# Performance work log

Hardware: AMD Instinct MI355X
Metric: run time of the kernel (lower is better)

Reference implementation:

```python
import jax, jax.numpy as jnp
import numpy as np

B, S, H = 8, 1024, 1024
NH, HD = 16, 64
EPS = 1e-12


def _p(w, g):
    # make_p_layer: w + gamma * clamp(w, min=0)
    return w + g * jnp.clip(w, 0.0, None)


def _pproc(x, W, b, g):
    # z = layer(x); zp = player(x); return zp * (z/zp).detach()  (value == z)
    z = x @ W.T + b
    zp = x @ _p(W, g).T + _p(b, g)
    return zp * jax.lax.stop_gradient(z / zp)


def _ln_nowb_detach(x):
    # 'nowb' LayerNorm (no weight/bias), mean and std detached (LNargsDetach)
    m = jax.lax.stop_gradient(jnp.mean(x, axis=-1, keepdims=True))
    v = jax.lax.stop_gradient(jnp.var(x, axis=-1, keepdims=True))
    return (x - m) / jnp.sqrt(v + EPS)


def setup_inputs() -> dict:
    key = jax.random.key(0)
    ks = jax.random.split(key, 10)
    lin = lambda k: (jax.random.normal(k, (H, H), jnp.float32) * 0.02)
    vec = lambda k: (jax.random.normal(k, (H,), jnp.float32) * 0.02)
    return {
        "hidden_states": jax.random.normal(ks[0], (B, S, H), jnp.float32),
        "Wq": lin(ks[1]), "bq": vec(ks[2]),
        "Wk": lin(ks[3]), "bk": vec(ks[4]),
        "Wv": lin(ks[5]), "bv": vec(ks[6]),
        "Wo": lin(ks[7]), "bo": vec(ks[8]),
        "gamma_AH": jnp.float32(0.1),
        "gamma_LN": jnp.float32(0.1),
    }


def reference(hidden_states, Wq, bq, Wk, bk, Wv, bv, Wo, bo, gamma_AH, gamma_LN):
    g = gamma_AH
    # dual-pass Q/K/V (pproc: value == plain linear, grads via perturbed layer)
    q = _pproc(hidden_states, Wq, bq, g)   # [B,S,H]
    k = _pproc(hidden_states, Wk, bk, g)
    v = _pproc(hidden_states, Wv, bv, g)
    split = lambda x: x.reshape(B, S, NH, HD).transpose(0, 2, 1, 3)  # [B,NH,S,HD]
    qt, kt, vt = split(q), split(k), split(v)
    # NOTE: original code does NOT scale by 1/sqrt(head_dim)
    scores = jnp.einsum('bhqd,bhkd->bhqk', qt, kt)
    attn = jax.nn.softmax(scores, axis=-1)
    probs = (1.0 - g) * jax.lax.stop_gradient(attn) + g * attn
    ctx = jnp.einsum('bhqk,bhkd->bhqd', probs, vt)
    ctx = ctx.transpose(0, 2, 1, 3).reshape(B, S, H)  # [B,S,H]
    # BertSelfOutput.pforward: perturbed dense (gamma_LN) + residual + detached LN
    h = ctx @ _p(Wo, gamma_LN).T + _p(bo, gamma_LN)
    out = _ln_nowb_detach(h + hidden_states)
    return out, probs
```

## Files before the change

kernel.cpp:

```cpp
#include <hip/hip_runtime.h>

typedef short short8 __attribute__((ext_vector_type(8)));
typedef float floatx4 __attribute__((ext_vector_type(4)));
typedef unsigned short ushort8v __attribute__((ext_vector_type(8)));

#define B_ 8
#define S_ 1024
#define H_ 1024
#define NH_ 16
#define HD_ 64

__device__ __forceinline__ unsigned short f2bf(float f) {
  unsigned u = __float_as_uint(f);
  u += 0x7fffu + ((u >> 16) & 1u);
  return (unsigned short)(u >> 16);
}

__device__ __forceinline__ floatx4 mfma16(short8 a, short8 b, floatx4 c) {
  return __builtin_amdgcn_mfma_f32_16x16x32_bf16(a, b, c, 0, 0, 0);
}

__device__ __forceinline__ void gload16(const void* g, void* lds) {
  __builtin_amdgcn_global_load_lds(
      (const __attribute__((address_space(1))) unsigned int*)g,
      (__attribute__((address_space(3))) unsigned int*)lds, 16, 0, 0);
}

__global__ void __launch_bounds__(256) cvt_x(const float* __restrict__ src,
                                             unsigned short* __restrict__ dst) {
  int i = (blockIdx.x * 256 + threadIdx.x) * 4;
  float4 v = *(const float4*)(src + i);
  ushort4 o;
  o.x = f2bf(v.x); o.y = f2bf(v.y); o.z = f2bf(v.z); o.w = f2bf(v.w);
  *(ushort4*)(dst + i) = o;
}

__global__ void __launch_bounds__(256) cvt_w(
    const float* __restrict__ W0, const float* __restrict__ W1,
    const float* __restrict__ W2, const float* __restrict__ W3,
    unsigned short* __restrict__ o0, unsigned short* __restrict__ o1,
    unsigned short* __restrict__ o2, unsigned short* __restrict__ o3,
    const float* __restrict__ gLN) {
  const int which = blockIdx.y;
  const float* src = (which == 0) ? W0 : (which == 1) ? W1 : (which == 2) ? W2 : W3;
  unsigned short* dst = (which == 0) ? o0 : (which == 1) ? o1 : (which == 2) ? o2 : o3;
  const float g = (which == 3) ? gLN[0] : 0.0f;
  int i = (blockIdx.x * 256 + threadIdx.x) * 4;
  float4 v = *(const float4*)(src + i);
  ushort4 o;
  o.x = f2bf(v.x + g * fmaxf(v.x, 0.f));
  o.y = f2bf(v.y + g * fmaxf(v.y, 0.f));
  o.z = f2bf(v.z + g * fmaxf(v.z, 0.f));
  o.w = f2bf(v.w + g * fmaxf(v.w, 0.f));
  *(ushort4*)(dst + i) = o;
}

__device__ __forceinline__ void gemm_mainloop(const unsigned short* __restrict__ Ag,
                                              const unsigned short* __restrict__ Bg,
                                              int K,
                                              unsigned short* As, unsigned short* Bs,
                                              floatx4 acc[4][4]) {
  const int tid = threadIdx.x;
  const int l = tid & 63, w = tid >> 6;
  const int l15 = l & 15, l4 = l >> 4;
  const int wm = (w & 1) << 6, wn = (w >> 1) << 6;
  const int srow = w * 32 + (l >> 2);
  const int scol = (l & 3) << 3;
  for (int k0 = 0; k0 < K; k0 += 32) {
    __syncthreads();
    gload16(&Ag[(size_t)srow * K + k0 + scol],        &As[srow * 32 + scol]);
    gload16(&Ag[(size_t)(srow + 16) * K + k0 + scol], &As[(srow + 16) * 32 + scol]);
    gload16(&Bg[(size_t)srow * K + k0 + scol],        &Bs[srow * 32 + scol]);
    gload16(&Bg[(size_t)(srow + 16) * K + k0 + scol], &Bs[(srow + 16) * 32 + scol]);
    __syncthreads();
    short8 a[4], bb[4];
#pragma unroll
    for (int i = 0; i < 4; ++i)
      a[i] = *(const short8*)&As[(wm + i * 16 + l15) * 32 + l4 * 8];
#pragma unroll
    for (int j = 0; j < 4; ++j)
      bb[j] = *(const short8*)&Bs[(wn + j * 16 + l15) * 32 + l4 * 8];
#pragma unroll
    for (int i = 0; i < 4; ++i)
#pragma unroll
      for (int j = 0; j < 4; ++j)
        acc[i][j] = mfma16(a[i], bb[j], acc[i][j]);
  }
}

__global__ void __launch_bounds__(256) gemm_qkv(
    const unsigned short* __restrict__ xb,
    const unsigned short* __restrict__ wq, const unsigned short* __restrict__ wk,
    const unsigned short* __restrict__ wv,
    const float* __restrict__ bq, const float* __restrict__ bk, const float* __restrict__ bv,
    unsigned short* __restrict__ oq, unsigned short* __restrict__ ok,
    unsigned short* __restrict__ ov) {
  __shared__ __align__(16) unsigned short As[128 * 32];
  __shared__ __align__(16) unsigned short Bs[128 * 32];
  const int z = blockIdx.z;
  const unsigned short* W = (z == 0) ? wq : (z == 1) ? wk : wv;
  const float* bias        = (z == 0) ? bq : (z == 1) ? bk : bv;
  unsigned short* O        = (z == 0) ? oq : (z == 1) ? ok : ov;
  const int nBase = blockIdx.x * 128, mBase = blockIdx.y * 128;
  floatx4 acc[4][4];
  const floatx4 fz = {0.f, 0.f, 0.f, 0.f};
#pragma unroll
  for (int i = 0; i < 4; ++i)
#pragma unroll
    for (int j = 0; j < 4; ++j) acc[i][j] = fz;
  gemm_mainloop(xb + (size_t)mBase * H_, W + (size_t)nBase * H_, H_, As, Bs, acc);
  const int l = threadIdx.x & 63, w = threadIdx.x >> 6;
  const int l15 = l & 15, l4 = l >> 4;
  const int wm = (w & 1) << 6, wn = (w >> 1) << 6;
#pragma unroll
  for (int i = 0; i < 4; ++i) {
    int row = mBase + wm + i * 16 + l4 * 4;
#pragma unroll
    for (int j = 0; j < 4; ++j) {
      int col = nBase + wn + j * 16 + l15;
      float bcol = bias[col];
#pragma unroll
      for (int r = 0; r < 4; ++r)
        O[(size_t)(row + r) * H_ + col] = f2bf(acc[i][j][r] + bcol);
    }
  }
}

__global__ void __launch_bounds__(256) transpose_v(const unsigned short* __restrict__ vb,
                                                   unsigned short* __restrict__ vt) {
  const int st = blockIdx.x, h = blockIdx.y, b = blockIdx.z;
  __shared__ __align__(16) unsigned short t[64 * 72];
  const int tid = threadIdx.x;
  const unsigned short* src = vb + (size_t)(b * S_ + st * 64) * H_ + h * HD_;
  for (int c = tid; c < 512; c += 256) {
    int i = c >> 3, dg = (c & 7) << 3;
    *(uint4*)&t[i * 72 + dg] = *(const uint4*)&src[(size_t)i * H_ + dg];
  }
  __syncthreads();
  unsigned short* dst = vt + ((size_t)(b * NH_ + h) * HD_) * S_ + st * 64;
  for (int c = tid; c < 512; c += 256) {
    int d = c >> 3, ig = (c & 7) << 3;
    ushort8v v;
#pragma unroll
    for (int ii = 0; ii < 8; ++ii) v[ii] = t[(ig + ii) * 72 + d];
    *(ushort8v*)&dst[(size_t)d * S_ + ig] = v;
  }
}

__global__ void __launch_bounds__(256) attn_kernel(
    const unsigned short* __restrict__ qg_, const unsigned short* __restrict__ kg_,
    const unsigned short* __restrict__ vtg_,
    float* __restrict__ probs, unsigned short* __restrict__ ctxb) {
  const int qt = blockIdx.x, h = blockIdx.y, b = blockIdx.z;
  __shared__ __align__(16) unsigned short Qs[64 * 64];
  __shared__ __align__(16) unsigned short Ks[128 * 64];
  __shared__ __align__(16) unsigned short Vts[64 * 128];
  __shared__ __align__(16) unsigned short Ps[64 * 128];
  const int tid = threadIdx.x;
  const int l = tid & 63, w = tid >> 6;
  const int l15 = l & 15, l4 = l >> 4;
  const int l7 = l & 7, lr8 = l >> 3;

  const unsigned short* qg = qg_ + ((size_t)(b * S_) + qt * 64) * H_ + h * HD_;
  const unsigned short* kg = kg_ + (size_t)(b * S_) * H_ + h * HD_;
  const unsigned short* vg = vtg_ + ((size_t)(b * NH_ + h) * HD_) * S_;

  const int kcol = (l7 ^ lr8) << 3;

#pragma unroll
  for (int c = 0; c < 2; ++c) {
    int row = w * 16 + c * 8 + lr8;
    gload16(&qg[(size_t)row * H_ + (l7 << 3)], &Qs[row * 64 + (l7 << 3)]);
  }
  __syncthreads();
  short8 aq0 = *(const short8*)&Qs[(w * 16 + l15) * 64 + l4 * 8];
  short8 aq1 = *(const short8*)&Qs[(w * 16 + l15) * 64 + 32 + l4 * 8];

  float esum[4] = {0.f, 0.f, 0.f, 0.f};
  for (int kt = 0; kt < 8; ++kt) {
    __syncthreads();
#pragma unroll
    for (int c = 0; c < 4; ++c) {
      int row = w * 32 + c * 8 + lr8;
      gload16(&kg[(size_t)(kt * 128 + row) * H_ + kcol], &Ks[row * 64 + (l7 << 3)]);
    }
    __syncthreads();
#pragma unroll
    for (int j = 0; j < 8; ++j) {
      int rr = l15 & 7;
      short8 b0 = *(const short8*)&Ks[(j * 16 + l15) * 64 + ((l4 ^ rr) << 3)];
      short8 b1 = *(const short8*)&Ks[(j * 16 + l15) * 64 + (((4 + l4) ^ rr) << 3)];
      floatx4 s = {0.f, 0.f, 0.f, 0.f};
      s = mfma16(aq0, b0, s);
      s = mfma16(aq1, b1, s);
#pragma unroll
      for (int r = 0; r < 4; ++r) esum[r] += __expf(s[r]);
    }
  }
#pragma unroll
  for (int m = 1; m < 16; m <<= 1)
#pragma unroll
    for (int r = 0; r < 4; ++r) esum[r] += __shfl_xor(esum[r], m, 64);
  float rinv[4];
#pragma unroll
  for (int r = 0; r < 4; ++r) rinv[r] = 1.0f / esum[r];

  const floatx4 fz = {0.f, 0.f, 0.f, 0.f};
  floatx4 cacc[4];
#pragma unroll
  for (int dt = 0; dt < 4; ++dt) cacc[dt] = fz;
  const int qrow_base = qt * 64 + w * 16 + l4 * 4;
  for (int kt = 0; kt < 8; ++kt) {
    __syncthreads();
#pragma unroll
    for (int c = 0; c < 4; ++c) {
      int row = w * 32 + c * 8 + lr8;
      gload16(&kg[(size_t)(kt * 128 + row) * H_ + kcol], &Ks[row * 64 + (l7 << 3)]);
    }
#pragma unroll
    for (int c = 0; c < 4; ++c) {
      int row = w * 16 + c * 4 + l4;
      int scol = (l15 ^ (c * 4 + l4)) << 3;
      gload16(&vg[(size_t)row * S_ + kt * 128 + scol], &Vts[row * 128 + (l15 << 3)]);
    }
    __syncthreads();
#pragma unroll
    for (int j = 0; j < 8; ++j) {
      int rr = l15 & 7;
      short8 b0 = *(const short8*)&Ks[(j * 16 + l15) * 64 + ((l4 ^ rr) << 3)];
      short8 b1 = *(const short8*)&Ks[(j * 16 + l15) * 64 + (((4 + l4) ^ rr) << 3)];
      floatx4 s = {0.f, 0.f, 0.f, 0.f};
      s = mfma16(aq0, b0, s);
      s = mfma16(aq1, b1, s);
      float* pp = probs + ((size_t)((b * NH_ + h) * S_) + qrow_base) * S_ + kt * 128 + j * 16 + l15;
#pragma unroll
      for (int r = 0; r < 4; ++r) {
        float p = __expf(s[r]) * rinv[r];
        pp[(size_t)r * S_] = p;
        int prow = w * 16 + l4 * 4 + r;
        int pslot = (j * 2 + (l15 >> 3)) ^ (l4 * 4 + r);
        Ps[prow * 128 + (pslot << 3) + (l15 & 7)] = f2bf(p);
      }
    }
    __syncthreads();
    short8 ap[4];
#pragma unroll
    for (int ks = 0; ks < 4; ++ks)
      ap[ks] = *(const short8*)&Ps[(w * 16 + l15) * 128 + (((ks * 4 + l4) ^ l15) << 3)];
#pragma unroll
    for (int dt = 0; dt < 4; ++dt)
#pragma unroll
      for (int ks = 0; ks < 4; ++ks) {
        short8 bv = *(const short8*)&Vts[(dt * 16 + l15) * 128 + (((ks * 4 + l4) ^ l15) << 3)];
        cacc[dt] = mfma16(ap[ks], bv, cacc[dt]);
      }
  }
  const int rowg = b * S_ + qt * 64 + w * 16 + l4 * 4;
#pragma unroll
  for (int dt = 0; dt < 4; ++dt)
#pragma unroll
    for (int r = 0; r < 4; ++r)
      ctxb[(size_t)(rowg + r) * H_ + h * HD_ + dt * 16 + l15] = f2bf(cacc[dt][r]);
}

__global__ void __launch_bounds__(256) gemm_out(
    const unsigned short* __restrict__ ctxb, const unsigned short* __restrict__ wob,
    const float* __restrict__ bo, const float* __restrict__ gln,
    const float* __restrict__ xres, float* __restrict__ hres) {
  __shared__ __align__(16) unsigned short As[128 * 32];
  __shared__ __align__(16) unsigned short Bs[128 * 32];
  const int nBase = blockIdx.x * 128, mBase = blockIdx.y * 128;
  floatx4 acc[4][4];
  const floatx4 fz = {0.f, 0.f, 0.f, 0.f};
#pragma unroll
  for (int i = 0; i < 4; ++i)
#pragma unroll
    for (int j = 0; j < 4; ++j) acc[i][j] = fz;
  gemm_mainloop(ctxb + (size_t)mBase * H_, wob + (size_t)nBase * H_, H_, As, Bs, acc);
  const float g = gln[0];
  const int l = threadIdx.x & 63, w = threadIdx.x >> 6;
  const int l15 = l & 15, l4 = l >> 4;
  const int wm = (w & 1) << 6, wn = (w >> 1) << 6;
#pragma unroll
  for (int i = 0; i < 4; ++i) {
    int row = mBase + wm + i * 16 + l4 * 4;
#pragma unroll
    for (int j = 0; j < 4; ++j) {
      int col = nBase + wn + j * 16 + l15;
      float pb = bo[col];
      pb += g * fmaxf(pb, 0.f);
#pragma unroll
      for (int r = 0; r < 4; ++r)
        hres[(size_t)(row + r) * H_ + col] =
            acc[i][j][r] + pb + xres[(size_t)(row + r) * H_ + col];
    }
  }
}

__global__ void __launch_bounds__(256) ln_kernel(const float* __restrict__ hres,
                                                 float* __restrict__ out) {
  const int row = blockIdx.x;
  const int tid = threadIdx.x;
  const float* xr = hres + (size_t)row * H_;
  float4 v = *(const float4*)&xr[tid * 4];
  float s = v.x + v.y + v.z + v.w;
  float q = v.x * v.x + v.y * v.y + v.z * v.z + v.w * v.w;
#pragma unroll
  for (int m = 1; m < 64; m <<= 1) {
    s += __shfl_xor(s, m, 64);
    q += __shfl_xor(q, m, 64);
  }
  __shared__ float sh[8];
  const int w = tid >> 6, l = tid & 63;
  if (l == 0) { sh[w] = s; sh[4 + w] = q; }
  __syncthreads();
  s = sh[0] + sh[1] + sh[2] + sh[3];
  q = sh[4] + sh[5] + sh[6] + sh[7];
  float mean = s * (1.f / 1024.f);
  float var = q * (1.f / 1024.f) - mean * mean;
  float inv = rsqrtf(var + 1e-12f);
  float4 o;
  o.x = (v.x - mean) * inv;
  o.y = (v.y - mean) * inv;
  o.z = (v.z - mean) * inv;
  o.w = (v.w - mean) * inv;
  *(float4*)&out[(size_t)row * H_ + tid * 4] = o;
}

extern "C" void kernel_launch(void* const* d_in, const int* in_sizes, int n_in,
                              void* d_out, int out_size, void* d_ws, size_t ws_size,
                              hipStream_t stream) {
  const float* x   = (const float*)d_in[0];
  const float* Wq  = (const float*)d_in[1];
  const float* bq  = (const float*)d_in[2];
  const float* Wk  = (const float*)d_in[3];
  const float* bk  = (const float*)d_in[4];
  const float* Wv  = (const float*)d_in[5];
  const float* bv  = (const float*)d_in[6];
  const float* Wo  = (const float*)d_in[7];
  const float* bo  = (const float*)d_in[8];
  const float* gLN = (const float*)d_in[10];

  float* out   = (float*)d_out;
  float* probs = out + (size_t)B_ * S_ * H_;

  unsigned short* xb  = (unsigned short*)d_ws;
  unsigned short* wqb = xb + 8388608;
  unsigned short* wkb = wqb + 1048576;
  unsigned short* wvb = wkb + 1048576;
  unsigned short* wob = wvb + 1048576;
  unsigned short* qb  = wob + 1048576;
  unsigned short* kb  = qb + 8388608;
  unsigned short* vb  = kb + 8388608;
  unsigned short* vt  = vb + 8388608;
  unsigned short* ctxb = xb;
  float* hres = (float*)qb;

  cvt_x<<<8192, 256, 0, stream>>>(x, xb);
  cvt_w<<<dim3(1024, 4), 256, 0, stream>>>(Wq, Wk, Wv, Wo, wqb, wkb, wvb, wob, gLN);

  gemm_qkv<<<dim3(8, 64, 3), 256, 0, stream>>>(xb, wqb, wkb, wvb, bq, bk, bv, qb, kb, vb);
  transpose_v<<<dim3(16, 16, 8), 256, 0, stream>>>(vb, vt);
  attn_kernel<<<dim3(16, 16, 8), 256, 0, stream>>>(qb, kb, vt, probs, ctxb);
  gemm_out<<<dim3(8, 64, 1), 256, 0, stream>>>(ctxb, wob, bo, gLN, x, hres);
  ln_kernel<<<8192, 256, 0, stream>>>(hres, out);
}
```

Before: 827.0 us.

## Single-pass attention caching exp scores in LDS, deferred normalization

Replaces the two-pass attention, which recomputed QK^T and exp, with a single pass. Unnormalized exp scores for the full 64x1024 row block are stored as bf16 in LDS (128KB), and P·V is accumulated from them while K/V tiles are prefetched with a double-buffered V. Normalization is applied once at the end to both ctx and the probs written out with vectorized float4 stores. The block grows to 512 threads. Risks include the large LDS footprint (one block per CU), and the probs output now being rounded through bf16 exp values rather than computed in fp32.

```diff
diff --git a/kernel.cpp b/kernel.cpp
--- a/kernel.cpp
+++ b/kernel.cpp
@@ -14,6 +14,10 @@
   unsigned u = __float_as_uint(f);
   u += 0x7fffu + ((u >> 16) & 1u);
   return (unsigned short)(u >> 16);
+}
+
+__device__ __forceinline__ float bf2f(unsigned short u) {
+  return __uint_as_float((unsigned)u << 16);
 }
 
 __device__ __forceinline__ floatx4 mfma16(short8 a, short8 b, floatx4 c) {
@@ -147,120 +151,137 @@
   }
 }
 
-__global__ void __launch_bounds__(256) attn_kernel(
+__global__ void __launch_bounds__(512) attn_kernel(
     const unsigned short* __restrict__ qg_, const unsigned short* __restrict__ kg_,
     const unsigned short* __restrict__ vtg_,
     float* __restrict__ probs, unsigned short* __restrict__ ctxb) {
   const int qt = blockIdx.x, h = blockIdx.y, b = blockIdx.z;
-  __shared__ __align__(16) unsigned short Qs[64 * 64];
-  __shared__ __align__(16) unsigned short Ks[128 * 64];
-  __shared__ __align__(16) unsigned short Vts[64 * 128];
-  __shared__ __align__(16) unsigned short Ps[64 * 128];
+  __shared__ __align__(16) unsigned short E[64 * 1024];
+  __shared__ __align__(16) unsigned short Ks[64 * 64];
+  __shared__ __align__(16) unsigned short Vb[2][64 * 64];
+  __shared__ float sh_esum[4 * 64];
+  __shared__ float sh_rinv[64];
   const int tid = threadIdx.x;
   const int l = tid & 63, w = tid >> 6;
   const int l15 = l & 15, l4 = l >> 4;
-  const int l7 = l & 7, lr8 = l >> 3;
+  const int j = w & 3;
+  const int wh = w >> 2;
 
   const unsigned short* qg = qg_ + ((size_t)(b * S_) + qt * 64) * H_ + h * HD_;
   const unsigned short* kg = kg_ + (size_t)(b * S_) * H_ + h * HD_;
   const unsigned short* vg = vtg_ + ((size_t)(b * NH_ + h) * HD_) * S_;
 
-  const int kcol = (l7 ^ lr8) << 3;
-
-#pragma unroll
-  for (int c = 0; c < 2; ++c) {
-    int row = w * 16 + c * 8 + lr8;
-    gload16(&qg[(size_t)row * H_ + (l7 << 3)], &Qs[row * 64 + (l7 << 3)]);
-  }
-  __syncthreads();
-  short8 aq0 = *(const short8*)&Qs[(w * 16 + l15) * 64 + l4 * 8];
-  short8 aq1 = *(const short8*)&Qs[(w * 16 + l15) * 64 + 32 + l4 * 8];
-
-  float esum[4] = {0.f, 0.f, 0.f, 0.f};
-  for (int kt = 0; kt < 8; ++kt) {
+  const int srow = tid >> 3;
+  const int sslot = (tid & 7) ^ (srow & 7);
+  gload16(&kg[(size_t)srow * H_ + (sslot << 3)], &Ks[(size_t)tid * 8]);
+  gload16(&vg[(size_t)srow * S_ + (sslot << 3)], &Vb[0][(size_t)tid * 8]);
+
+  short8 aq[2][2];
+#pragma unroll
+  for (int rg2 = 0; rg2 < 2; ++rg2)
+#pragma unroll
+    for (int hh = 0; hh < 2; ++hh)
+      aq[rg2][hh] = *(const short8*)&qg[(size_t)(wh * 32 + rg2 * 16 + l15) * H_ + hh * 32 + l4 * 8];
+
+  const floatx4 fz = {0.f, 0.f, 0.f, 0.f};
+  float es[2][4] = {{0.f, 0.f, 0.f, 0.f}, {0.f, 0.f, 0.f, 0.f}};
+  floatx4 cacc[2];
+  cacc[0] = fz; cacc[1] = fz;
+
+  for (int kt = 0; kt < 16; ++kt) {
     __syncthreads();
-#pragma unroll
-    for (int c = 0; c < 4; ++c) {
-      int row = w * 32 + c * 8 + lr8;
-      gload16(&kg[(size_t)(kt * 128 + row) * H_ + kcol], &Ks[row * 64 + (l7 << 3)]);
+    const int krow = j * 16 + l15;
+    const int kb7 = krow & 7;
+    short8 bk0 = *(const short8*)&Ks[krow * 64 + ((l4 ^ kb7) << 3)];
+    short8 bk1 = *(const short8*)&Ks[krow * 64 + (((4 + l4) ^ kb7) << 3)];
+#pragma unroll
+    for (int rg2 = 0; rg2 < 2; ++rg2) {
+      floatx4 s = fz;
+      s = mfma16(aq[rg2][0], bk0, s);
+      s = mfma16(aq[rg2][1], bk1, s);
+      const int rowb = wh * 32 + rg2 * 16 + l4 * 4;
+      const int cs = kt * 8 + j * 2 + (l15 >> 3);
+#pragma unroll
+      for (int r = 0; r < 4; ++r) {
+        float e = __expf(s[r]);
+        es[rg2][r] += e;
+        const int row = rowb + r;
+        E[row * 1024 + ((cs ^ (row & 7)) << 3) + (l15 & 7)] = f2bf(e);
+      }
     }
     __syncthreads();
-#pragma unroll
-    for (int j = 0; j < 8; ++j) {
-      int rr = l15 & 7;
-      short8 b0 = *(const short8*)&Ks[(j * 16 + l15) * 64 + ((l4 ^ rr) << 3)];
-      short8 b1 = *(const short8*)&Ks[(j * 16 + l15) * 64 + (((4 + l4) ^ rr) << 3)];
-      floatx4 s = {0.f, 0.f, 0.f, 0.f};
-      s = mfma16(aq0, b0, s);
-      s = mfma16(aq1, b1, s);
-#pragma unroll
-      for (int r = 0; r < 4; ++r) esum[r] += __expf(s[r]);
-    }
-  }
-#pragma unroll
-  for (int m = 1; m < 16; m <<= 1)
-#pragma unroll
-    for (int r = 0; r < 4; ++r) esum[r] += __shfl_xor(esum[r], m, 64);
-  float rinv[4];
-#pragma unroll
-  for (int r = 0; r < 4; ++r) rinv[r] = 1.0f / esum[r];
-
-  const floatx4 fz = {0.f, 0.f, 0.f, 0.f};
-  floatx4 cacc[4];
-#pragma unroll
-  for (int dt = 0; dt < 4; ++dt) cacc[dt] = fz;
-  const int qrow_base = qt * 64 + w * 16 + l4 * 4;
-  for (int kt = 0; kt < 8; ++kt) {
-    __syncthreads();
-#pragma unroll
-    for (int c = 0; c < 4; ++c) {
-      int row = w * 32 + c * 8 + lr8;
-      gload16(&kg[(size_t)(kt * 128 + row) * H_ + kcol], &Ks[row * 64 + (l7 << 3)]);
-    }
-#pragma unroll
-    for (int c = 0; c < 4; ++c) {
-      int row = w * 16 + c * 4 + l4;
-      int scol = (l15 ^ (c * 4 + l4)) << 3;
-      gload16(&vg[(size_t)row * S_ + kt * 128 + scol], &Vts[row * 128 + (l15 << 3)]);
-    }
-    __syncthreads();
-#pragma unroll
-    for (int j = 0; j < 8; ++j) {
-      int rr = l15 & 7;
-      short8 b0 = *(const short8*)&Ks[(j * 16 + l15) * 64 + ((l4 ^ rr) << 3)];
-      short8 b1 = *(const short8*)&Ks[(j * 16 + l15) * 64 + (((4 + l4) ^ rr) << 3)];
-      floatx4 s = {0.f, 0.f, 0.f, 0.f};
-      s = mfma16(aq0, b0, s);
-      s = mfma16(aq1, b1, s);
-      float* pp = probs + ((size_t)((b * NH_ + h) * S_) + qrow_base) * S_ + kt * 128 + j * 16 + l15;
-#pragma unroll
-      for (int r = 0; r < 4; ++r) {
-        float p = __expf(s[r]) * rinv[r];
-        pp[(size_t)r * S_] = p;
-        int prow = w * 16 + l4 * 4 + r;
-        int pslot = (j * 2 + (l15 >> 3)) ^ (l4 * 4 + r);
-        Ps[prow * 128 + (pslot << 3) + (l15 & 7)] = f2bf(p);
-      }
-    }
-    __syncthreads();
-    short8 ap[4];
-#pragma unroll
-    for (int ks = 0; ks < 4; ++ks)
-      ap[ks] = *(const short8*)&Ps[(w * 16 + l15) * 128 + (((ks * 4 + l4) ^ l15) << 3)];
-#pragma unroll
-    for (int dt = 0; dt < 4; ++dt)
-#pragma unroll
-      for (int ks = 0; ks < 4; ++ks) {
-        short8 bv = *(const short8*)&Vts[(dt * 16 + l15) * 128 + (((ks * 4 + l4) ^ l15) << 3)];
-        cacc[dt] = mfma16(ap[ks], bv, cacc[dt]);
-      }
-  }
-  const int rowg = b * S_ + qt * 64 + w * 16 + l4 * 4;
-#pragma unroll
-  for (int dt = 0; dt < 4; ++dt)
+    if (kt < 15) {
+      gload16(&kg[(size_t)((kt + 1) * 64 + srow) * H_ + (sslot << 3)], &Ks[(size_t)tid * 8]);
+      gload16(&vg[(size_t)srow * S_ + (kt + 1) * 64 + (sslot << 3)],
+              &Vb[(kt + 1) & 1][(size_t)tid * 8]);
+    }
+    const int prow = j * 16 + l15;
+    const int p7 = prow & 7;
+    const unsigned short* Vc = Vb[kt & 1];
+    short8 ap0 = *(const short8*)&E[prow * 1024 + (((kt * 8 + l4) ^ p7) << 3)];
+    short8 ap1 = *(const short8*)&E[prow * 1024 + (((kt * 8 + 4 + l4) ^ p7) << 3)];
+#pragma unroll
+    for (int dt = 0; dt < 2; ++dt) {
+      const int d = wh * 32 + dt * 16 + l15;
+      const int d7 = d & 7;
+      short8 bv0 = *(const short8*)&Vc[d * 64 + ((l4 ^ d7) << 3)];
+      short8 bv1 = *(const short8*)&Vc[d * 64 + (((4 + l4) ^ d7) << 3)];
+      cacc[dt] = mfma16(ap0, bv0, cacc[dt]);
+      cacc[dt] = mfma16(ap1, bv1, cacc[dt]);
+    }
+  }
+
+  __syncthreads();
+#pragma unroll
+  for (int rg2 = 0; rg2 < 2; ++rg2)
 #pragma unroll
     for (int r = 0; r < 4; ++r)
-      ctxb[(size_t)(rowg + r) * H_ + h * HD_ + dt * 16 + l15] = f2bf(cacc[dt][r]);
+#pragma unroll
+      for (int m = 1; m < 16; m <<= 1)
+        es[rg2][r] += __shfl_xor(es[rg2][r], m, 64);
+  if (l15 == 0) {
+#pragma unroll
+    for (int rg2 = 0; rg2 < 2; ++rg2)
+#pragma unroll
+      for (int r = 0; r < 4; ++r)
+        sh_esum[j * 64 + wh * 32 + rg2 * 16 + l4 * 4 + r] = es[rg2][r];
+  }
+  __syncthreads();
+  if (tid < 64)
+    sh_rinv[tid] = 1.0f / (sh_esum[tid] + sh_esum[64 + tid] +
+                           sh_esum[128 + tid] + sh_esum[192 + tid]);
+  __syncthreads();
+
+  const size_t pbase = ((size_t)((b * NH_ + h) * S_) + qt * 64) * S_;
+#pragma unroll 4
+  for (int it = 0; it < 16; ++it) {
+    const int lin = it * 512 + tid;
+    const int row = lin >> 7, sl = lin & 127;
+    short8 ev = *(const short8*)&E[row * 1024 + ((sl ^ (row & 7)) << 3)];
+    const float rv = sh_rinv[row];
+    float* dst = probs + pbase + (size_t)row * S_ + sl * 8;
+    float4 o0, o1;
+    o0.x = bf2f((unsigned short)ev[0]) * rv;
+    o0.y = bf2f((unsigned short)ev[1]) * rv;
+    o0.z = bf2f((unsigned short)ev[2]) * rv;
+    o0.w = bf2f((unsigned short)ev[3]) * rv;
+    o1.x = bf2f((unsigned short)ev[4]) * rv;
+    o1.y = bf2f((unsigned short)ev[5]) * rv;
+    o1.z = bf2f((unsigned short)ev[6]) * rv;
+    o1.w = bf2f((unsigned short)ev[7]) * rv;
+    *(float4*)dst = o0;
+    *(float4*)(dst + 4) = o1;
+  }
+
+  const int rowg = b * S_ + qt * 64 + j * 16 + l4 * 4;
+#pragma unroll
+  for (int dt = 0; dt < 2; ++dt)
+#pragma unroll
+    for (int r = 0; r < 4; ++r) {
+      const float rv = sh_rinv[j * 16 + l4 * 4 + r];
+      ctxb[(size_t)(rowg + r) * H_ + h * HD_ + wh * 32 + dt * 16 + l15] =
+          f2bf(cacc[dt][r] * rv);
+    }
 }
 
 __global__ void __launch_bounds__(256) gemm_out(
@@ -361,7 +382,7 @@
 
   gemm_qkv<<<dim3(8, 64, 3), 256, 0, stream>>>(xb, wqb, wkb, wvb, bq, bk, bv, qb, kb, vb);
   transpose_v<<<dim3(16, 16, 8), 256, 0, stream>>>(vb, vt);
-  attn_kernel<<<dim3(16, 16, 8), 256, 0, stream>>>(qb, kb, vt, probs, ctxb);
+  attn_kernel<<<dim3(16, 16, 8), 512, 0, stream>>>(qb, kb, vt, probs, ctxb);
   gemm_out<<<dim3(8, 64, 1), 256, 0, stream>>>(ctxb, wob, bo, gLN, x, hres);
   ln_kernel<<<8192, 256, 0, stream>>>(hres, out);
 }
```

After: 888.6 us. 1.07x slower.
